# Kernel tuning notes

Measured on AMD Instinct MI355X. Metric: run time of the kernel, lower is better.

## Reference

```python
import jax, jax.numpy as jnp
import numpy as np

T = 2048      # sequence length
V = 100000    # vocab size
E = 256       # embedding dim
H2 = 256      # hidden per direction (hidden_dim // 2)
L = 32        # number of labels
CLS = 0
SEP = 31
NEG = -10000.0


def setup_inputs() -> dict:
    key = jax.random.key(0)
    ks = jax.random.split(key, 16)
    s = 0.1
    inp = {}
    inp["input_ids"] = jax.random.randint(ks[0], (T,), 0, V, dtype=jnp.int32)
    inp["attention_mask"] = jnp.ones((T,), dtype=jnp.int32)
    inp["target"] = jax.random.randint(ks[1], (T,), 0, L, dtype=jnp.int32)
    # learned params
    inp["emb"] = jax.random.normal(ks[2], (V, E), jnp.float32) * s
    inp["w_ih_f"] = jax.random.normal(ks[3], (4 * H2, E), jnp.float32) * s
    inp["w_hh_f"] = jax.random.normal(ks[4], (4 * H2, H2), jnp.float32) * s
    inp["b_f"] = jax.random.normal(ks[5], (4 * H2,), jnp.float32) * s  # b_ih + b_hh fused
    inp["w_ih_b"] = jax.random.normal(ks[6], (4 * H2, E), jnp.float32) * s
    inp["w_hh_b"] = jax.random.normal(ks[7], (4 * H2, H2), jnp.float32) * s
    inp["b_b"] = jax.random.normal(ks[8], (4 * H2,), jnp.float32) * s
    inp["w_lin"] = jax.random.normal(ks[9], (L, 2 * H2), jnp.float32) * s
    inp["b_lin"] = jax.random.normal(ks[10], (L,), jnp.float32) * s
    trans = jax.random.normal(ks[11], (L, L), jnp.float32)
    trans = trans.at[CLS, :].set(NEG).at[:, SEP].set(NEG)
    inp["trans"] = trans
    inp["h0"] = jax.random.normal(ks[12], (2, H2), jnp.float32)  # [fwd/bwd, H2]
    inp["c0"] = jax.random.normal(ks[13], (2, H2), jnp.float32)
    return inp


def _lstm_dir(x, h0, c0, w_ih, w_hh, b, reverse):
    # x: [T, E] -> hidden states [T, H2]; torch gate order i, f, g, o
    def step(carry, xt):
        h, c = carry
        z = xt @ w_ih.T + h @ w_hh.T + b
        i, f, g, o = jnp.split(z, 4)
        i = jax.nn.sigmoid(i)
        f = jax.nn.sigmoid(f)
        g = jnp.tanh(g)
        o = jax.nn.sigmoid(o)
        c = f * c + i * g
        h = o * jnp.tanh(c)
        return (h, c), h
    _, hs = jax.lax.scan(step, (h0, c0), x, reverse=reverse)
    return hs


def _crf_neg_log_likelihood(logits, trans, target):
    # partition function via forward algorithm (vectorized over tag pairs)
    alpha0 = jnp.full((L,), NEG, logits.dtype).at[CLS].set(0.0)
    def crf_step(alpha, emit):
        # alpha_new[next] = logsumexp_prev(alpha[prev] + trans[next, prev]) + emit[next]
        alpha = jax.nn.logsumexp(alpha[None, :] + trans, axis=1) + emit
        return alpha, None
    alpha, _ = jax.lax.scan(crf_step, alpha0, logits)
    forward_score = jax.nn.logsumexp(alpha + trans[SEP])
    # gold path score
    tags = jnp.concatenate([jnp.array([CLS], dtype=target.dtype), target])
    trans_score = jnp.sum(trans[tags[1:], tags[:-1]]) + trans[SEP, tags[-1]]
    emit_score = jnp.sum(jnp.take_along_axis(logits, tags[1:, None], axis=1))
    return forward_score - (trans_score + emit_score)


def reference(input_ids, attention_mask, target, emb, w_ih_f, w_hh_f, b_f,
              w_ih_b, w_hh_b, b_b, w_lin, b_lin, trans, h0, c0):
    x = emb[input_ids]                                   # [T, E]
    hf = _lstm_dir(x, h0[0], c0[0], w_ih_f, w_hh_f, b_f, False)
    hb = _lstm_dir(x, h0[1], c0[1], w_ih_b, w_hh_b, b_b, True)
    hs = jnp.concatenate([hf, hb], axis=-1)              # [T, 2*H2]
    logits = hs @ w_lin.T + b_lin                        # [T, L]
    return _crf_neg_log_likelihood(logits, trans, target)
```

## Files before the change

kernel.cpp:

```cpp
#include <hip/hip_runtime.h>
#include <hip/hip_bf16.h>
#include <cstddef>

#define T_LEN 2048
#define H2 256
#define G4 1024
#define NLBL 32
#define CLS_TAG 0
#define SEP_TAG 31


#if defined(__has_builtin)
#if __has_builtin(__builtin_amdgcn_sdot8)
#define HAS_SDOT8 1
#endif
#if __has_builtin(__builtin_amdgcn_rcpf)
#define HAS_RCPF 1
#endif
#if __has_builtin(__builtin_amdgcn_mov_dpp)
#define HAS_MOVDPP 1
#endif
#endif

__device__ __forceinline__ void dot8(int& acc, int a, int b) {
#if defined(HAS_SDOT8)
    acc = __builtin_amdgcn_sdot8(a, b, acc, false);
#elif defined(__gfx950__) || defined(__gfx942__) || defined(__gfx90a__)
    asm("v_dot8_i32_i4 %0, %1, %2, %0" : "+v"(acc) : "v"(a), "v"(b));
#else
    #pragma unroll
    for (int m = 0; m < 8; ++m) {
        int av = (a << (28 - 4 * m)) >> 28;
        int bv = (b << (28 - 4 * m)) >> 28;
        acc += av * bv;
    }
#endif
}

__device__ __forceinline__ void pin_v(int& x) {
    asm volatile("" : "+v"(x));
}

__device__ __forceinline__ float rcpf(float x) {
#ifdef HAS_RCPF
    return __builtin_amdgcn_rcpf(x);
#else
    return 1.0f / x;
#endif
}

__device__ __forceinline__ float sigf(float x) {
    return rcpf(1.0f + __expf(-x));
}

__device__ __forceinline__ float tanhf_(float x) {
    x = fminf(fmaxf(x, -15.0f), 15.0f);
    float e = __expf(2.0f * x);
    return (e - 1.0f) * rcpf(e + 1.0f);
}

__device__ __forceinline__ int xchg_xor1(int x) {
#if defined(HAS_MOVDPP)
    return __builtin_amdgcn_mov_dpp(x, 0xB1, 0xF, 0xF, true);
#else
    return __shfl_xor(x, 1, 64);
#endif
}

__device__ __forceinline__ int xchg_xor2(int x) {
#if defined(HAS_MOVDPP)
    return __builtin_amdgcn_mov_dpp(x, 0x4E, 0xF, 0xF, true);
#else
    return __shfl_xor(x, 2, 64);
#endif
}


__global__ __launch_bounds__(256) void gather_k(const int* __restrict__ ids,
                                                const float* __restrict__ emb,
                                                float* __restrict__ xbuf) {
    int t = blockIdx.x;
    int row = ids[t];
    xbuf[(size_t)t * 256 + threadIdx.x] = emb[(size_t)row * 256 + threadIdx.x];
}

__global__ __launch_bounds__(256) void quant_w_k(const float* __restrict__ w_hh_f,
                                                 const float* __restrict__ w_hh_b,
                                                 unsigned int* __restrict__ wq4,
                                                 float* __restrict__ srowP) {
    int wave = threadIdx.x >> 6, lane = threadIdx.x & 63;
    int rg = blockIdx.x * 4 + wave;
    int dir = rg >> 10, m = rg & 1023;
    int g = m >> 8, u = m & 255;
    const float* src = (dir ? w_hh_b : w_hh_f) + (size_t)m * H2;
    float4 w4 = ((const float4*)src)[lane];
    float mx = fmaxf(fmaxf(fabsf(w4.x), fabsf(w4.y)), fmaxf(fabsf(w4.z), fabsf(w4.w)));
    #pragma unroll
    for (int off = 32; off; off >>= 1) mx = fmaxf(mx, __shfl_xor(mx, off, 64));
    float s = (mx > 0.0f) ? mx * (1.0f / 7.0f) : 1.0f;
    float inv = (mx > 0.0f) ? 7.0f * rcpf(mx) : 0.0f;
    int q0 = __float2int_rn(w4.x * inv);
    int q1 = __float2int_rn(w4.y * inv);
    int q2 = __float2int_rn(w4.z * inv);
    int q3 = __float2int_rn(w4.w * inv);
    unsigned int half = (unsigned)(q0 & 15) | ((unsigned)(q1 & 15) << 4) |
                        ((unsigned)(q2 & 15) << 8) | ((unsigned)(q3 & 15) << 12);
    unsigned int other = (unsigned int)__shfl_xor((int)half, 1, 64);
    if ((lane & 1) == 0)
        wq4[(size_t)((dir * 256 + u) * 4 + g) * 32 + (lane >> 1)] = half | (other << 16);
    if (lane == 0) srowP[(dir * 256 + u) * 4 + g] = s;
}

__global__ __launch_bounds__(64) void quant_h0_k(const float* __restrict__ h0,
                                                 unsigned int* __restrict__ hq0,
                                                 float* __restrict__ sh0) {
    int dir = blockIdx.x, lane = threadIdx.x;
    float4 h4 = ((const float4*)(h0 + (size_t)dir * H2))[lane];
    float mx = fmaxf(fmaxf(fabsf(h4.x), fabsf(h4.y)), fmaxf(fabsf(h4.z), fabsf(h4.w)));
    #pragma unroll
    for (int off = 32; off; off >>= 1) mx = fmaxf(mx, __shfl_xor(mx, off, 64));
    float s = (mx > 0.0f) ? mx * (1.0f / 7.0f) : 1.0f;
    float inv = (mx > 0.0f) ? 7.0f * rcpf(mx) : 0.0f;
    int q0 = __float2int_rn(h4.x * inv);
    int q1 = __float2int_rn(h4.y * inv);
    int q2 = __float2int_rn(h4.z * inv);
    int q3 = __float2int_rn(h4.w * inv);
    unsigned int half = (unsigned)(q0 & 15) | ((unsigned)(q1 & 15) << 4) |
                        ((unsigned)(q2 & 15) << 8) | ((unsigned)(q3 & 15) << 12);
    unsigned int other = (unsigned int)__shfl_xor((int)half, 1, 64);
    if ((lane & 1) == 0)
        hq0[dir * 32 + (lane >> 1)] = half | (other << 16);
    if (lane == 0) sh0[dir] = s;
}

__global__ __launch_bounds__(256) void gemm_xproj_k(const float* __restrict__ xbuf,
                                                    const float* __restrict__ w_ih_f,
                                                    const float* __restrict__ w_ih_b,
                                                    const float* __restrict__ b_f,
                                                    const float* __restrict__ b_b,
                                                    float* __restrict__ xprojP) {
    __shared__ float As[64][33];
    __shared__ float Bs[64][33];
    int tid = threadIdx.x;
    int t0 = blockIdx.x * 64;
    int n0 = blockIdx.y * 64;
    int tx = tid & 15, ty = tid >> 4;
    float acc[4][4] = {};
    for (int k0 = 0; k0 < 256; k0 += 32) {
        #pragma unroll
        for (int i = 0; i < 8; ++i) {
            int idx = tid + i * 256;
            int r = idx >> 5, kk = idx & 31;
            As[r][kk] = xbuf[(size_t)(t0 + r) * 256 + k0 + kk];
            int nn = n0 + r;
            const float* wsrc = (nn < 1024) ? (w_ih_f + (size_t)nn * 256)
                                            : (w_ih_b + (size_t)(nn - 1024) * 256);
            Bs[r][kk] = wsrc[k0 + kk];
        }
        __syncthreads();
        #pragma unroll
        for (int kk = 0; kk < 32; ++kk) {
            float a[4], b[4];
            #pragma unroll
            for (int i = 0; i < 4; ++i) a[i] = As[ty * 4 + i][kk];
            #pragma unroll
            for (int j = 0; j < 4; ++j) b[j] = Bs[tx * 4 + j][kk];
            #pragma unroll
            for (int i = 0; i < 4; ++i)
                #pragma unroll
                for (int j = 0; j < 4; ++j) acc[i][j] += a[i] * b[j];
        }
        __syncthreads();
    }
    #pragma unroll
    for (int j = 0; j < 4; ++j) {
        int nn = n0 + tx * 4 + j;
        int dir = nn >> 10, nl = nn & 1023;
        float bias = dir ? b_b[nl] : b_f[nl];
        int pidx = (nl & 255) * 4 + (nl >> 8);
        #pragma unroll
        for (int i = 0; i < 4; ++i) {
            int t = t0 + ty * 4 + i;
            xprojP[((size_t)dir * T_LEN + t) * G4 + pidx] = acc[i][j] + bias;
        }
    }
}

__global__ __launch_bounds__(256, 1) void lstm_rec_k(const unsigned int* __restrict__ wq4,
                                                     const float* __restrict__ srowP,
                                                     const float* __restrict__ xprojP,
                                                     const unsigned int* __restrict__ hq0,
                                                     const float* __restrict__ sh0v,
                                                     const float* __restrict__ c0,
                                                     float* __restrict__ hs) {
    const int dir = blockIdx.x;
    const int u = threadIdx.x;
    __shared__ __align__(16) unsigned int hqs[2][32];

    int w0[32], w1[32], w2[32], w3[32];
    {
        const unsigned int* wr = wq4 + (size_t)(dir * 256 + u) * 128;
        #pragma unroll
        for (int j = 0; j < 32; ++j) { w0[j] = (int)wr[j];      pin_v(w0[j]); }
        #pragma unroll
        for (int j = 0; j < 32; ++j) { w1[j] = (int)wr[32 + j]; pin_v(w1[j]); }
        #pragma unroll
        for (int j = 0; j < 32; ++j) { w2[j] = (int)wr[64 + j]; pin_v(w2[j]); }
        #pragma unroll
        for (int j = 0; j < 32; ++j) { w3[j] = (int)wr[96 + j]; pin_v(w3[j]); }
    }
    float4 sr4 = ((const float4*)srowP)[dir * 256 + u];
    float sh0 = sh0v[dir];
    float c = c0[dir * H2 + u];
    const float4* xp4 = (const float4*)(xprojP + (size_t)dir * T_LEN * G4);

    float4 scS = make_float4(sr4.x * (1.0f / 7.0f), sr4.y * (1.0f / 7.0f),
                             sr4.z * (1.0f / 7.0f), sr4.w * (1.0f / 7.0f));
    float4 scA = make_float4(sr4.x * sh0, sr4.y * sh0, sr4.z * sh0, sr4.w * sh0);

    if (u < 32) hqs[0][u] = hq0[dir * 32 + u];

    const int stp = dir ? -1 : 1;
    const int ts0 = dir ? (T_LEN - 1) : 0;
    const long zstep = (long)stp * 256;
    const long hstep = (long)stp * 512;

    const float4* pz = xp4 + (size_t)ts0 * 256 + u;
    float4 zx = pz[0];
    float4 zb = pz[zstep];
    const float4* pp = pz + 2 * zstep;
    float* hp = hs + (size_t)ts0 * 512 + dir * H2 + u;
    __syncthreads();

    auto body = [&](const unsigned int* rdbuf, unsigned int* wrbuf,
                    const float4& sc) __attribute__((always_inline)) {
        int hv[32];
        #pragma unroll
        for (int jq = 0; jq < 8; ++jq) {
            int4 q = ((const int4*)rdbuf)[jq];
            hv[4 * jq + 0] = q.x; hv[4 * jq + 1] = q.y;
            hv[4 * jq + 2] = q.z; hv[4 * jq + 3] = q.w;
        }
        float4 zc = *pp; pp += zstep;

        int a0 = 0, a1 = 0, a2 = 0, a3 = 0;
        #pragma unroll
        for (int j = 0; j < 32; ++j) {
            dot8(a0, w0[j], hv[j]);
            dot8(a1, w1[j], hv[j]);
            dot8(a2, w2[j], hv[j]);
            dot8(a3, w3[j], hv[j]);
        }
        float zi = zx.x + sc.x * (float)a0;
        float zf = zx.y + sc.y * (float)a1;
        float zg = zx.z + sc.z * (float)a2;
        float zo = zx.w + sc.w * (float)a3;
        float ig = sigf(zi), fg = sigf(zf), gg = tanhf_(zg), og = sigf(zo);
        c = fg * c + ig * gg;
        float h = og * tanhf_(c);
        int qv = __float2int_rn(fminf(fmaxf(h * 7.0f, -7.0f), 7.0f));
        int nib = qv & 15;
        int pn = xchg_xor1(nib);
        int b01 = (nib | (pn << 4)) & 255;
        int b23 = xchg_xor2(b01);
        if ((u & 3) == 0)
            ((unsigned short*)&wrbuf[0])[u >> 2] =
                (unsigned short)((b01 | (b23 << 8)) & 0xFFFF);
        *hp = h; hp += hstep;
        zx = zb; zb = zc;
        asm volatile("s_waitcnt lgkmcnt(0)" ::: "memory");
        __builtin_amdgcn_s_barrier();
        __builtin_amdgcn_sched_barrier(0);
    };

    body(hqs[0], hqs[1], scA);
    for (int it = 0; it < 1023; ++it) {
        body(hqs[1], hqs[0], scS);
        body(hqs[0], hqs[1], scS);
    }
    body(hqs[1], hqs[0], scS);
}

__global__ __launch_bounds__(128) void logits_k(const float* __restrict__ hs,
                                                const float* __restrict__ w_lin,
                                                const float* __restrict__ b_lin,
                                                float* __restrict__ logits) {
    __shared__ float wldT[512][17];
    __shared__ float hld[8][512];
    int tid = threadIdx.x;
    int t0 = blockIdx.x * 8;
    int n0 = blockIdx.y * 16;
    for (int i = tid; i < 16 * 512; i += 128) {
        int j = i >> 9, k = i & 511;
        wldT[k][j] = w_lin[(size_t)(n0 + j) * 512 + k];
    }
    for (int i = tid; i < 8 * 512; i += 128) {
        int tq = i >> 9, k = i & 511;
        hld[tq][k] = hs[(size_t)(t0 + tq) * 512 + k];
    }
    __syncthreads();
    int j = tid & 15, tq = tid >> 4;
    float acc = b_lin[n0 + j];
    #pragma unroll 8
    for (int k = 0; k < 512; ++k) acc += hld[tq][k] * wldT[k][j];
    logits[(size_t)(t0 + tq) * NLBL + n0 + j] = acc;
}

__global__ __launch_bounds__(256) void gold_k(const float* __restrict__ trans,
                                              const int* __restrict__ target,
                                              const float* __restrict__ logits,
                                              float* __restrict__ gold) {
    __shared__ float red[256];
    int tid = threadIdx.x;
    float s = 0.0f;
    for (int t = tid; t < T_LEN; t += 256) {
        int cur = target[t];
        int prev = (t == 0) ? CLS_TAG : target[t - 1];
        s += trans[cur * NLBL + prev] + logits[(size_t)t * NLBL + cur];
    }
    if (tid == 0) s += trans[SEP_TAG * NLBL + target[T_LEN - 1]];
    red[tid] = s;
    __syncthreads();
    for (int st = 128; st; st >>= 1) {
        if (tid < st) red[tid] += red[tid + st];
        __syncthreads();
    }
    if (tid == 0) gold[0] = red[0];
}

__global__ __launch_bounds__(1024) void crf_chain0_k(const float* __restrict__ logits,
                                                     const float* __restrict__ trans,
                                                     float* __restrict__ mats) {
    const int tid = threadIdx.x;
    const int n = tid >> 5, p = tid & 31;
    __shared__ float Rl[2][NLBL][NLBL + 1];
    __shared__ float tl[NLBL][NLBL + 1];
    const int t0 = blockIdx.x * 8;
    float e[8];
    #pragma unroll
    for (int s = 0; s < 8; ++s) e[s] = logits[(size_t)(t0 + s) * NLBL + n];
    float myt = trans[n * NLBL + p];
    tl[n][p] = myt;
    __syncthreads();
    float tr[NLBL];
    #pragma unroll
    for (int k = 0; k < NLBL; ++k) tr[k] = tl[n][k];
    Rl[0][n][p] = myt + e[0];
    __syncthreads();
    float rn = 0.0f;
    for (int s = 1; s < 8; ++s) {
        const int cur = (s - 1) & 1, nxt = s & 1;
        float v[NLBL];
        #pragma unroll
        for (int k = 0; k < NLBL; ++k) v[k] = tr[k] + Rl[cur][k][p];
        float m = v[0];
        #pragma unroll
        for (int k = 1; k < NLBL; ++k) m = fmaxf(m, v[k]);
        float sum = 0.0f;
        #pragma unroll
        for (int k = 0; k < NLBL; ++k) sum += __expf(v[k] - m);
        rn = e[s] + m + __logf(sum);
        Rl[nxt][n][p] = rn;
        __syncthreads();
    }
    mats[(size_t)blockIdx.x * 1024 + tid] = rn;
}

__global__ __launch_bounds__(1024) void crf_chainN_k(const float* __restrict__ min_,
                                                     float* __restrict__ mout,
                                                     int chunk) {
    const int tid = threadIdx.x;
    const int n = tid >> 5, p = tid & 31;
    __shared__ float Rl[2][NLBL][NLBL + 1];
    __shared__ float Al[2][NLBL][NLBL + 1];
    const size_t base = (size_t)blockIdx.x * chunk;
    float rn = min_[base * 1024 + tid];
    Rl[0][n][p] = rn;
    float anext = min_[(base + 1) * 1024 + tid];
    __syncthreads();
    for (int s = 1; s < chunk; ++s) {
        const int cur = (s - 1) & 1, nxt = s & 1;
        Al[nxt][n][p] = anext;
        if (s + 1 < chunk) anext = min_[(base + s + 1) * 1024 + tid];
        __syncthreads();
        float v[NLBL];
        #pragma unroll
        for (int k = 0; k < NLBL; ++k) v[k] = Al[nxt][n][k] + Rl[cur][k][p];
        float m = v[0];
        #pragma unroll
        for (int k = 1; k < NLBL; ++k) m = fmaxf(m, v[k]);
        float sum = 0.0f;
        #pragma unroll
        for (int k = 0; k < NLBL; ++k) sum += __expf(v[k] - m);
        rn = m + __logf(sum);
        Rl[nxt][n][p] = rn;
        __syncthreads();
    }
    mout[(size_t)blockIdx.x * 1024 + tid] = rn;
}

__global__ __launch_bounds__(1024) void crf_finish_k(const float* __restrict__ min_,
                                                     const float* __restrict__ trans,
                                                     const float* __restrict__ gold,
                                                     float* __restrict__ out,
                                                     int chunk) {
    const int tid = threadIdx.x;
    const int n = tid >> 5, p = tid & 31;
    __shared__ float Rl[2][NLBL][NLBL + 1];
    __shared__ float Al[2][NLBL][NLBL + 1];
    __shared__ float af[NLBL];
    float rn = min_[tid];
    Rl[0][n][p] = rn;
    float anext = min_[1024 + tid];
    __syncthreads();
    for (int s = 1; s < chunk; ++s) {
        const int cur = (s - 1) & 1, nxt = s & 1;
        Al[nxt][n][p] = anext;
        if (s + 1 < chunk) anext = min_[(size_t)(s + 1) * 1024 + tid];
        __syncthreads();
        float v[NLBL];
        #pragma unroll
        for (int k = 0; k < NLBL; ++k) v[k] = Al[nxt][n][k] + Rl[cur][k][p];
        float m = v[0];
        #pragma unroll
        for (int k = 1; k < NLBL; ++k) m = fmaxf(m, v[k]);
        float sum = 0.0f;
        #pragma unroll
        for (int k = 0; k < NLBL; ++k) sum += __expf(v[k] - m);
        rn = m + __logf(sum);
        Rl[nxt][n][p] = rn;
        __syncthreads();
    }
    float val = rn + ((p == CLS_TAG) ? 0.0f : -10000.0f);
    float m = val;
    #pragma unroll
    for (int off = 16; off; off >>= 1) m = fmaxf(m, __shfl_xor(m, off, 32));
    float esum = __expf(val - m);
    #pragma unroll
    for (int off = 16; off; off >>= 1) esum += __shfl_xor(esum, off, 32);
    if (p == 0) af[n] = m + __logf(esum);
    __syncthreads();
    if (tid < NLBL) {
        float f = af[tid] + trans[SEP_TAG * NLBL + tid];
        float mm = f;
        #pragma unroll
        for (int off = 16; off; off >>= 1) mm = fmaxf(mm, __shfl_xor(mm, off, 32));
        float es = __expf(f - mm);
        #pragma unroll
        for (int off = 16; off; off >>= 1) es += __shfl_xor(es, off, 32);
        if (tid == 0) out[0] = mm + __logf(es) - gold[0];
    }
}


extern "C" void kernel_launch(void* const* d_in, const int* in_sizes, int n_in,
                              void* d_out, int out_size, void* d_ws, size_t ws_size,
                              hipStream_t stream) {
    const int*   ids     = (const int*)d_in[0];
    const int*   target  = (const int*)d_in[2];
    const float* emb     = (const float*)d_in[3];
    const float* w_ih_f  = (const float*)d_in[4];
    const float* w_hh_f  = (const float*)d_in[5];
    const float* b_f     = (const float*)d_in[6];
    const float* w_ih_b  = (const float*)d_in[7];
    const float* w_hh_b  = (const float*)d_in[8];
    const float* b_b     = (const float*)d_in[9];
    const float* w_lin   = (const float*)d_in[10];
    const float* b_lin   = (const float*)d_in[11];
    const float* trans   = (const float*)d_in[12];
    const float* h0      = (const float*)d_in[13];
    const float* c0      = (const float*)d_in[14];
    float* out = (float*)d_out;

    char* ws = (char*)d_ws;
    size_t off = 0;
    float* xbuf   = (float*)(ws + off); off += (size_t)T_LEN * 256 * 4;
    float* xprojP = (float*)(ws + off); off += (size_t)2 * T_LEN * G4 * 4;
    float* hs     = (float*)(ws + off); off += (size_t)T_LEN * 512 * 4;
    float* logits = (float*)(ws + off); off += (size_t)T_LEN * NLBL * 4;
    float* srowP  = (float*)(ws + off); off += (size_t)2 * G4 * 4;
    float* sh0v   = (float*)(ws + off); off += 16;
    float* gold   = (float*)(ws + off); off += 16;
    unsigned int* hq0 = (unsigned int*)(ws + off); off += (size_t)2 * 32 * 4;
    unsigned int* wq4 = (unsigned int*)(ws + off); off += (size_t)2 * G4 * 32 * 4;
    float* mats1 = xbuf;
    float* mats2 = xbuf + 256 * 1024;

    gather_k<<<T_LEN, 256, 0, stream>>>(ids, emb, xbuf);
    quant_w_k<<<512, 256, 0, stream>>>(w_hh_f, w_hh_b, wq4, srowP);
    quant_h0_k<<<2, 64, 0, stream>>>(h0, hq0, sh0v);
    gemm_xproj_k<<<dim3(32, 32), 256, 0, stream>>>(xbuf, w_ih_f, w_ih_b, b_f, b_b, xprojP);
    lstm_rec_k<<<2, 256, 0, stream>>>(wq4, srowP, xprojP, hq0, sh0v, c0, hs);
    logits_k<<<dim3(256, 2), 128, 0, stream>>>(hs, w_lin, b_lin, logits);
    gold_k<<<1, 256, 0, stream>>>(trans, target, logits, gold);
    crf_chain0_k<<<256, 1024, 0, stream>>>(logits, trans, mats1);
    crf_chainN_k<<<16, 1024, 0, stream>>>(mats1, mats2, 16);
    crf_finish_k<<<1, 1024, 0, stream>>>(mats2, trans, gold, out, 16);
}
```

Before: 1.272 ms.

## Merge prep kernels into one launch and simplify recurrent h nibble packing

Combines the embedding gather, recurrent weight quantization and h0 quantization kernels into a single launch that dispatches on block index, removing two kernel launches. In the recurrent step, the quantized h nibble pairs are now written to LDS as bytes by every even lane instead of exchanging a second time and writing 16-bit values from every fourth lane. This drops one DPP exchange from the serial critical path but doubles the number of lanes doing LDS stores. The fp32 h store is also moved earlier in the step.

```diff
diff --git a/kernel.cpp b/kernel.cpp
--- a/kernel.cpp
+++ b/kernel.cpp
@@ -67,70 +67,68 @@
 #endif
 }
 
-__device__ __forceinline__ int xchg_xor2(int x) {
-#if defined(HAS_MOVDPP)
-    return __builtin_amdgcn_mov_dpp(x, 0x4E, 0xF, 0xF, true);
-#else
-    return __shfl_xor(x, 2, 64);
-#endif
-}
-
-
-__global__ __launch_bounds__(256) void gather_k(const int* __restrict__ ids,
-                                                const float* __restrict__ emb,
-                                                float* __restrict__ xbuf) {
-    int t = blockIdx.x;
-    int row = ids[t];
-    xbuf[(size_t)t * 256 + threadIdx.x] = emb[(size_t)row * 256 + threadIdx.x];
-}
-
-__global__ __launch_bounds__(256) void quant_w_k(const float* __restrict__ w_hh_f,
-                                                 const float* __restrict__ w_hh_b,
-                                                 unsigned int* __restrict__ wq4,
-                                                 float* __restrict__ srowP) {
-    int wave = threadIdx.x >> 6, lane = threadIdx.x & 63;
-    int rg = blockIdx.x * 4 + wave;
-    int dir = rg >> 10, m = rg & 1023;
-    int g = m >> 8, u = m & 255;
-    const float* src = (dir ? w_hh_b : w_hh_f) + (size_t)m * H2;
-    float4 w4 = ((const float4*)src)[lane];
-    float mx = fmaxf(fmaxf(fabsf(w4.x), fabsf(w4.y)), fmaxf(fabsf(w4.z), fabsf(w4.w)));
-    #pragma unroll
-    for (int off = 32; off; off >>= 1) mx = fmaxf(mx, __shfl_xor(mx, off, 64));
-    float s = (mx > 0.0f) ? mx * (1.0f / 7.0f) : 1.0f;
-    float inv = (mx > 0.0f) ? 7.0f * rcpf(mx) : 0.0f;
-    int q0 = __float2int_rn(w4.x * inv);
-    int q1 = __float2int_rn(w4.y * inv);
-    int q2 = __float2int_rn(w4.z * inv);
-    int q3 = __float2int_rn(w4.w * inv);
-    unsigned int half = (unsigned)(q0 & 15) | ((unsigned)(q1 & 15) << 4) |
-                        ((unsigned)(q2 & 15) << 8) | ((unsigned)(q3 & 15) << 12);
-    unsigned int other = (unsigned int)__shfl_xor((int)half, 1, 64);
-    if ((lane & 1) == 0)
-        wq4[(size_t)((dir * 256 + u) * 4 + g) * 32 + (lane >> 1)] = half | (other << 16);
-    if (lane == 0) srowP[(dir * 256 + u) * 4 + g] = s;
-}
-
-__global__ __launch_bounds__(64) void quant_h0_k(const float* __restrict__ h0,
-                                                 unsigned int* __restrict__ hq0,
-                                                 float* __restrict__ sh0) {
-    int dir = blockIdx.x, lane = threadIdx.x;
-    float4 h4 = ((const float4*)(h0 + (size_t)dir * H2))[lane];
-    float mx = fmaxf(fmaxf(fabsf(h4.x), fabsf(h4.y)), fmaxf(fabsf(h4.z), fabsf(h4.w)));
-    #pragma unroll
-    for (int off = 32; off; off >>= 1) mx = fmaxf(mx, __shfl_xor(mx, off, 64));
-    float s = (mx > 0.0f) ? mx * (1.0f / 7.0f) : 1.0f;
-    float inv = (mx > 0.0f) ? 7.0f * rcpf(mx) : 0.0f;
-    int q0 = __float2int_rn(h4.x * inv);
-    int q1 = __float2int_rn(h4.y * inv);
-    int q2 = __float2int_rn(h4.z * inv);
-    int q3 = __float2int_rn(h4.w * inv);
-    unsigned int half = (unsigned)(q0 & 15) | ((unsigned)(q1 & 15) << 4) |
-                        ((unsigned)(q2 & 15) << 8) | ((unsigned)(q3 & 15) << 12);
-    unsigned int other = (unsigned int)__shfl_xor((int)half, 1, 64);
-    if ((lane & 1) == 0)
-        hq0[dir * 32 + (lane >> 1)] = half | (other << 16);
-    if (lane == 0) sh0[dir] = s;
+
+__global__ __launch_bounds__(256) void prep_k(const int* __restrict__ ids,
+                                              const float* __restrict__ emb,
+                                              float* __restrict__ xbuf,
+                                              const float* __restrict__ w_hh_f,
+                                              const float* __restrict__ w_hh_b,
+                                              unsigned int* __restrict__ wq4,
+                                              float* __restrict__ srowP,
+                                              const float* __restrict__ h0,
+                                              unsigned int* __restrict__ hq0,
+                                              float* __restrict__ sh0) {
+    const int b = blockIdx.x;
+    if (b < T_LEN) {
+        int row = ids[b];
+        xbuf[(size_t)b * 256 + threadIdx.x] = emb[(size_t)row * 256 + threadIdx.x];
+        return;
+    }
+    if (b < T_LEN + 512) {
+        int wave = threadIdx.x >> 6, lane = threadIdx.x & 63;
+        int rg = (b - T_LEN) * 4 + wave;
+        int dir = rg >> 10, m = rg & 1023;
+        int g = m >> 8, u = m & 255;
+        const float* src = (dir ? w_hh_b : w_hh_f) + (size_t)m * H2;
+        float4 w4 = ((const float4*)src)[lane];
+        float mx = fmaxf(fmaxf(fabsf(w4.x), fabsf(w4.y)), fmaxf(fabsf(w4.z), fabsf(w4.w)));
+        #pragma unroll
+        for (int off = 32; off; off >>= 1) mx = fmaxf(mx, __shfl_xor(mx, off, 64));
+        float s = (mx > 0.0f) ? mx * (1.0f / 7.0f) : 1.0f;
+        float inv = (mx > 0.0f) ? 7.0f * rcpf(mx) : 0.0f;
+        int q0 = __float2int_rn(w4.x * inv);
+        int q1 = __float2int_rn(w4.y * inv);
+        int q2 = __float2int_rn(w4.z * inv);
+        int q3 = __float2int_rn(w4.w * inv);
+        unsigned int half = (unsigned)(q0 & 15) | ((unsigned)(q1 & 15) << 4) |
+                            ((unsigned)(q2 & 15) << 8) | ((unsigned)(q3 & 15) << 12);
+        unsigned int other = (unsigned int)__shfl_xor((int)half, 1, 64);
+        if ((lane & 1) == 0)
+            wq4[(size_t)((dir * 256 + u) * 4 + g) * 32 + (lane >> 1)] = half | (other << 16);
+        if (lane == 0) srowP[(dir * 256 + u) * 4 + g] = s;
+        return;
+    }
+    {
+        int wave = threadIdx.x >> 6, lane = threadIdx.x & 63;
+        if (wave >= 2) return;
+        int dir = wave;
+        float4 h4 = ((const float4*)(h0 + (size_t)dir * H2))[lane];
+        float mx = fmaxf(fmaxf(fabsf(h4.x), fabsf(h4.y)), fmaxf(fabsf(h4.z), fabsf(h4.w)));
+        #pragma unroll
+        for (int off = 32; off; off >>= 1) mx = fmaxf(mx, __shfl_xor(mx, off, 64));
+        float s = (mx > 0.0f) ? mx * (1.0f / 7.0f) : 1.0f;
+        float inv = (mx > 0.0f) ? 7.0f * rcpf(mx) : 0.0f;
+        int q0 = __float2int_rn(h4.x * inv);
+        int q1 = __float2int_rn(h4.y * inv);
+        int q2 = __float2int_rn(h4.z * inv);
+        int q3 = __float2int_rn(h4.w * inv);
+        unsigned int half = (unsigned)(q0 & 15) | ((unsigned)(q1 & 15) << 4) |
+                            ((unsigned)(q2 & 15) << 8) | ((unsigned)(q3 & 15) << 12);
+        unsigned int other = (unsigned int)__shfl_xor((int)half, 1, 64);
+        if ((lane & 1) == 0)
+            hq0[dir * 32 + (lane >> 1)] = half | (other << 16);
+        if (lane == 0) sh0[dir] = s;
+    }
 }
 
 __global__ __launch_bounds__(256) void gemm_xproj_k(const float* __restrict__ xbuf,
@@ -258,15 +256,13 @@
         float ig = sigf(zi), fg = sigf(zf), gg = tanhf_(zg), og = sigf(zo);
         c = fg * c + ig * gg;
         float h = og * tanhf_(c);
+        *hp = h; hp += hstep;
         int qv = __float2int_rn(fminf(fmaxf(h * 7.0f, -7.0f), 7.0f));
         int nib = qv & 15;
         int pn = xchg_xor1(nib);
-        int b01 = (nib | (pn << 4)) & 255;
-        int b23 = xchg_xor2(b01);
-        if ((u & 3) == 0)
-            ((unsigned short*)&wrbuf[0])[u >> 2] =
-                (unsigned short)((b01 | (b23 << 8)) & 0xFFFF);
-        *hp = h; hp += hstep;
+        if ((u & 1) == 0)
+            ((unsigned char*)&wrbuf[0])[u >> 1] =
+                (unsigned char)((nib | (pn << 4)) & 255);
         zx = zb; zb = zc;
         asm volatile("s_waitcnt lgkmcnt(0)" ::: "memory");
         __builtin_amdgcn_s_barrier();
@@ -486,9 +482,9 @@
     float* mats1 = xbuf;
     float* mats2 = xbuf + 256 * 1024;
 
-    gather_k<<<T_LEN, 256, 0, stream>>>(ids, emb, xbuf);
-    quant_w_k<<<512, 256, 0, stream>>>(w_hh_f, w_hh_b, wq4, srowP);
-    quant_h0_k<<<2, 64, 0, stream>>>(h0, hq0, sh0v);
+    prep_k<<<T_LEN + 512 + 1, 256, 0, stream>>>(ids, emb, xbuf,
+                                                w_hh_f, w_hh_b, wq4, srowP,
+                                                h0, hq0, sh0v);
     gemm_xproj_k<<<dim3(32, 32), 256, 0, stream>>>(xbuf, w_ih_f, w_ih_b, b_f, b_b, xprojP);
     lstm_rec_k<<<2, 256, 0, stream>>>(wq4, srowP, xprojP, hq0, sh0v, c0, hs);
     logits_k<<<dim3(256, 2), 128, 0, stream>>>(hs, w_lin, b_lin, logits);
```

Result: no change. 1.269 ms (-0.3%).
